# Optimization experiments

Hardware: AMD Instinct MI355X
Metric: run time of the kernel (lower is better)

## Reference

```python
import jax, jax.numpy as jnp
import numpy as np

WINDOW_SIZE = 11
SIGMA = 1.5
C3 = 1e-4
EPS = 1e-12


def _gaussian_window(channels):
    # 1D Gaussian, normalized, then outer product -> 2D separable window
    coords = jnp.arange(WINDOW_SIZE, dtype=jnp.float32) - WINDOW_SIZE // 2
    g = jnp.exp(-coords ** 2 / (2.0 * SIGMA ** 2))
    g = g / g.sum()
    w2 = g[:, None] * g[None, :]                      # [K, K]
    return jnp.broadcast_to(w2, (channels, 1, WINDOW_SIZE, WINDOW_SIZE))


def _dwconv(x, w, channels):
    # depthwise (groups=C) 2D conv with SAME-style symmetric zero padding
    pad = WINDOW_SIZE // 2
    return jax.lax.conv_general_dilated(
        x, w,
        window_strides=(1, 1),
        padding=[(pad, pad), (pad, pad)],
        dimension_numbers=('NCHW', 'OIHW', 'NCHW'),
        feature_group_count=channels,
    )


def reference(x, y):
    x = x.astype(jnp.float32)
    y = y.astype(jnp.float32)
    N, C = x.shape[0], x.shape[1]
    w = _gaussian_window(C)
    mu_x = _dwconv(x, w, C)
    mu_y = _dwconv(y, w, C)
    sigma_xy = _dwconv(x * y, w, C) - mu_x * mu_y
    sigma_x = jnp.clip(_dwconv(x * x, w, C) - mu_x * mu_x, EPS, None)
    sigma_y = jnp.clip(_dwconv(y * y, w, C) - mu_y * mu_y, EPS, None)
    structure = (sigma_xy + C3) / (jnp.sqrt(sigma_x) * jnp.sqrt(sigma_y) + C3)
    structure_mean = structure.reshape(N, C, -1).mean(axis=2)  # [N, C]
    loss = (1.0 - structure_mean).mean()
    return loss


def setup_inputs() -> dict:
    key = jax.random.key(0)
    kx, ky = jax.random.split(key)
    x = jax.random.uniform(kx, (8, 3, 512, 512), dtype=jnp.float32)
    y = jax.random.uniform(ky, (8, 3, 512, 512), dtype=jnp.float32)
    return {"x": x, "y": y}
```

## Files before the change

### kernel.cpp

```cpp
#include <hip/hip_runtime.h>

#define IMG 512
#define ROWS 8
#define NITER 18
#define NPLANES 24
#define TOTAL_PIX 6291456.0f
#define NBLOCKS (64 * 24)

__device__ __constant__ float GW[11] = {
    0.00102838f, 0.00759876f, 0.03600050f, 0.10935817f, 0.21300535f,
    0.26601172f, 0.21300535f, 0.10935817f, 0.03600050f, 0.00759876f,
    0.00102838f};

#define VSTRIDE 264
#define QSTRIDE 528
#define LDS_F2 2640

extern "C" __global__ __launch_bounds__(256, 4) void ssim_structure_kernel(
    const float* __restrict__ x, const float* __restrict__ y,
    float* __restrict__ partial) {
  const int tid = threadIdx.x;
  const int chunk = blockIdx.x;
  const int plane = blockIdx.y;
  const int r0 = chunk * ROWS;

  const size_t pbase = (size_t)plane * (IMG * IMG / 2);
  const float2* __restrict__ xp = (const float2*)x + pbase;
  const float2* __restrict__ yp = (const float2*)y + pbase;

  __shared__ float2 vbuf[LDS_F2];
  for (int j = tid; j < LDS_F2; j += 256) vbuf[j] = make_float2(0.f, 0.f);
  __syncthreads();

  float bx0[11], bx1[11], by0[11], by1[11];
  float acc = 0.0f;

  auto loadrow = [&](int i, float2& ox, float2& oy) {
    const int ir = r0 - 5 + i;
    if (i < NITER && ir >= 0 && ir < IMG) {
      const size_t off = (size_t)ir * (IMG / 2) + tid;
      ox = xp[off];
      oy = yp[off];
    } else {
      ox = make_float2(0.f, 0.f);
      oy = make_float2(0.f, 0.f);
    }
  };

#pragma unroll
  for (int i = 0; i < 10; ++i) {
    float2 vx, vy;
    loadrow(i, vx, vy);
    bx0[i] = vx.x;
    bx1[i] = vx.y;
    by0[i] = vy.x;
    by1[i] = vy.y;
  }
  float2 px, py;
  loadrow(10, px, py);

#pragma unroll
  for (int j = 0; j < ROWS; ++j) {
    const int slot = (10 + j) % 11;
    const int sel = j & 1;
    bx0[slot] = px.x;
    bx1[slot] = px.y;
    by0[slot] = py.x;
    by1[slot] = py.y;
    loadrow(11 + j, px, py);

    float Vx0 = 0.f, Vx1 = 0.f, Vy0 = 0.f, Vy1 = 0.f;
    float Vxx0 = 0.f, Vxx1 = 0.f, Vyy0 = 0.f, Vyy1 = 0.f;
    float Vxy0 = 0.f, Vxy1 = 0.f;
#pragma unroll
    for (int k = 0; k < 11; ++k) {
      const int s = (j + k) % 11;
      const float wgt = GW[k];
      const float wx0 = wgt * bx0[s], wx1 = wgt * bx1[s];
      const float wy0 = wgt * by0[s], wy1 = wgt * by1[s];
      Vx0 += wx0;
      Vx1 += wx1;
      Vy0 += wy0;
      Vy1 += wy1;
      Vxx0 = fmaf(wx0, bx0[s], Vxx0);
      Vxx1 = fmaf(wx1, bx1[s], Vxx1);
      Vxy0 = fmaf(wx0, by0[s], Vxy0);
      Vxy1 = fmaf(wx1, by1[s], Vxy1);
      Vyy0 = fmaf(wy0, by0[s], Vyy0);
      Vyy1 = fmaf(wy1, by1[s], Vyy1);
    }
    const int wbase = sel * VSTRIDE + 3 + tid;
    vbuf[0 * QSTRIDE + wbase] = make_float2(Vx0, Vx1);
    vbuf[1 * QSTRIDE + wbase] = make_float2(Vy0, Vy1);
    vbuf[2 * QSTRIDE + wbase] = make_float2(Vxx0, Vxx1);
    vbuf[3 * QSTRIDE + wbase] = make_float2(Vyy0, Vyy1);
    vbuf[4 * QSTRIDE + wbase] = make_float2(Vxy0, Vxy1);
    __syncthreads();

    float S0[5], S1[5];
#pragma unroll
    for (int q = 0; q < 5; ++q) {
      const float2* arr = vbuf + q * QSTRIDE + sel * VSTRIDE + tid;
      float a[14];
#pragma unroll
      for (int d = 0; d < 7; ++d) {
        const float2 v = arr[d];
        a[2 * d] = v.x;
        a[2 * d + 1] = v.y;
      }
      float s0 = 0.f, s1 = 0.f;
#pragma unroll
      for (int d = 0; d < 11; ++d) {
        s0 = fmaf(GW[d], a[d + 1], s0);
        s1 = fmaf(GW[d], a[d + 2], s1);
      }
      S0[q] = s0;
      S1[q] = s1;
    }
    {
      const float mx = S0[0], my = S0[1];
      const float sxy = fmaf(-mx, my, S0[4]);
      const float sxx = fmaxf(fmaf(-mx, mx, S0[2]), 1e-12f);
      const float syy = fmaxf(fmaf(-my, my, S0[3]), 1e-12f);
      const float den = __builtin_amdgcn_sqrtf(sxx * syy) + 1e-4f;
      acc += (sxy + 1e-4f) * __builtin_amdgcn_rcpf(den);
    }
    {
      const float mx = S1[0], my = S1[1];
      const float sxy = fmaf(-mx, my, S1[4]);
      const float sxx = fmaxf(fmaf(-mx, mx, S1[2]), 1e-12f);
      const float syy = fmaxf(fmaf(-my, my, S1[3]), 1e-12f);
      const float den = __builtin_amdgcn_sqrtf(sxx * syy) + 1e-4f;
      acc += (sxy + 1e-4f) * __builtin_amdgcn_rcpf(den);
    }
  }

#pragma unroll
  for (int off = 32; off > 0; off >>= 1) acc += __shfl_down(acc, off, 64);
  __shared__ float wsum[4];
  if ((tid & 63) == 0) wsum[tid >> 6] = acc;
  __syncthreads();
  if (tid == 0) {
    partial[blockIdx.y * 64 + blockIdx.x] = wsum[0] + wsum[1] + wsum[2] + wsum[3];
  }
}

extern "C" __global__ void ssim_finalize_kernel(const float* __restrict__ partial,
                                                float* __restrict__ out) {
  const int tid = threadIdx.x;
  float s = 0.f;
  for (int j = tid; j < NBLOCKS; j += 256) s += partial[j];
#pragma unroll
  for (int off = 32; off > 0; off >>= 1) s += __shfl_down(s, off, 64);
  __shared__ float wsum[4];
  if ((tid & 63) == 0) wsum[tid >> 6] = s;
  __syncthreads();
  if (tid == 0) {
    out[0] = 1.0f - (wsum[0] + wsum[1] + wsum[2] + wsum[3]) * (1.0f / TOTAL_PIX);
  }
}

extern "C" void kernel_launch(void* const* d_in, const int* in_sizes, int n_in,
                              void* d_out, int out_size, void* d_ws,
                              size_t ws_size, hipStream_t stream) {
  const float* x = (const float*)d_in[0];
  const float* y = (const float*)d_in[1];
  float* out = (float*)d_out;
  float* partial = (float*)d_ws;

  dim3 grid(IMG / ROWS, NPLANES, 1);
  ssim_structure_kernel<<<grid, 256, 0, stream>>>(x, y, partial);
  ssim_finalize_kernel<<<1, 256, 0, stream>>>(partial, out);
}
```

Before: 134.6 us.

## Double rows per block, pack LDS intermediates as float4, inline weights

Each block now processes 16 output rows instead of 8, which halves the number of blocks and lowers the fraction of redundant halo row loads. The vertical-pass results are packed into float4/float2 LDS arrays so the horizontal pass issues wider, fewer LDS reads. Gaussian weights become compile-time constants instead of constant-memory loads. The full manual unroll over 16 rows raises code size and register pressure, and halving the grid gives the GPU less parallelism to spread across its compute units.

```diff
diff --git a/kernel.cpp b/kernel.cpp
--- a/kernel.cpp
+++ b/kernel.cpp
@@ -1,20 +1,89 @@
 #include <hip/hip_runtime.h>
 
 #define IMG 512
-#define ROWS 8
-#define NITER 18
+#define ROWS 16
+#define NITER 26
 #define NPLANES 24
 #define TOTAL_PIX 6291456.0f
-#define NBLOCKS (64 * 24)
-
-__device__ __constant__ float GW[11] = {
+#define NBLOCKS (32 * 24)
+
+constexpr float GW[11] = {
     0.00102838f, 0.00759876f, 0.03600050f, 0.10935817f, 0.21300535f,
     0.26601172f, 0.21300535f, 0.10935817f, 0.03600050f, 0.00759876f,
     0.00102838f};
 
-#define VSTRIDE 264
-#define QSTRIDE 528
-#define LDS_F2 2640
+__device__ __forceinline__ void vcol(
+    float x0, float x1, float x2, float x3, float x4, float x5, float x6,
+    float x7, float x8, float x9, float x10,
+    float y0, float y1, float y2, float y3, float y4, float y5, float y6,
+    float y7, float y8, float y9, float y10,
+    float& Vx, float& Vy, float& Vxx, float& Vyy, float& Vxy) {
+  Vx = 0.f; Vy = 0.f; Vxx = 0.f; Vyy = 0.f; Vxy = 0.f;
+#define VK(K)                                            \
+  {                                                      \
+    const float wx = GW[K] * x##K, wy = GW[K] * y##K;    \
+    Vx += wx;                                            \
+    Vy += wy;                                            \
+    Vxx = fmaf(wx, x##K, Vxx);                           \
+    Vxy = fmaf(wx, y##K, Vxy);                           \
+    Vyy = fmaf(wy, y##K, Vyy);                           \
+  }
+  VK(0) VK(1) VK(2) VK(3) VK(4) VK(5) VK(6) VK(7) VK(8) VK(9) VK(10)
+#undef VK
+}
+
+__device__ __forceinline__ void hconv4(
+    const float4 p0, const float4 p1, const float4 p2, const float4 p3,
+    const float4 p4, const float4 p5, const float4 p6,
+    float& s0a, float& s1a, float& s0b, float& s1b) {
+  s0a = GW[0] * p0.y;
+  s0a = fmaf(GW[1], p1.x, s0a); s0a = fmaf(GW[2], p1.y, s0a);
+  s0a = fmaf(GW[3], p2.x, s0a); s0a = fmaf(GW[4], p2.y, s0a);
+  s0a = fmaf(GW[5], p3.x, s0a); s0a = fmaf(GW[6], p3.y, s0a);
+  s0a = fmaf(GW[7], p4.x, s0a); s0a = fmaf(GW[8], p4.y, s0a);
+  s0a = fmaf(GW[9], p5.x, s0a); s0a = fmaf(GW[10], p5.y, s0a);
+  s1a = GW[0] * p1.x;
+  s1a = fmaf(GW[1], p1.y, s1a); s1a = fmaf(GW[2], p2.x, s1a);
+  s1a = fmaf(GW[3], p2.y, s1a); s1a = fmaf(GW[4], p3.x, s1a);
+  s1a = fmaf(GW[5], p3.y, s1a); s1a = fmaf(GW[6], p4.x, s1a);
+  s1a = fmaf(GW[7], p4.y, s1a); s1a = fmaf(GW[8], p5.x, s1a);
+  s1a = fmaf(GW[9], p5.y, s1a); s1a = fmaf(GW[10], p6.x, s1a);
+  s0b = GW[0] * p0.w;
+  s0b = fmaf(GW[1], p1.z, s0b); s0b = fmaf(GW[2], p1.w, s0b);
+  s0b = fmaf(GW[3], p2.z, s0b); s0b = fmaf(GW[4], p2.w, s0b);
+  s0b = fmaf(GW[5], p3.z, s0b); s0b = fmaf(GW[6], p3.w, s0b);
+  s0b = fmaf(GW[7], p4.z, s0b); s0b = fmaf(GW[8], p4.w, s0b);
+  s0b = fmaf(GW[9], p5.z, s0b); s0b = fmaf(GW[10], p5.w, s0b);
+  s1b = GW[0] * p1.z;
+  s1b = fmaf(GW[1], p1.w, s1b); s1b = fmaf(GW[2], p2.z, s1b);
+  s1b = fmaf(GW[3], p2.w, s1b); s1b = fmaf(GW[4], p3.z, s1b);
+  s1b = fmaf(GW[5], p3.w, s1b); s1b = fmaf(GW[6], p4.z, s1b);
+  s1b = fmaf(GW[7], p4.w, s1b); s1b = fmaf(GW[8], p5.z, s1b);
+  s1b = fmaf(GW[9], p5.w, s1b); s1b = fmaf(GW[10], p6.z, s1b);
+}
+
+__device__ __forceinline__ void hconv2(
+    const float2 q0, const float2 q1, const float2 q2, const float2 q3,
+    const float2 q4, const float2 q5, const float2 q6, float& s0, float& s1) {
+  s0 = GW[0] * q0.y;
+  s0 = fmaf(GW[1], q1.x, s0); s0 = fmaf(GW[2], q1.y, s0);
+  s0 = fmaf(GW[3], q2.x, s0); s0 = fmaf(GW[4], q2.y, s0);
+  s0 = fmaf(GW[5], q3.x, s0); s0 = fmaf(GW[6], q3.y, s0);
+  s0 = fmaf(GW[7], q4.x, s0); s0 = fmaf(GW[8], q4.y, s0);
+  s0 = fmaf(GW[9], q5.x, s0); s0 = fmaf(GW[10], q5.y, s0);
+  s1 = GW[0] * q1.x;
+  s1 = fmaf(GW[1], q1.y, s1); s1 = fmaf(GW[2], q2.x, s1);
+  s1 = fmaf(GW[3], q2.y, s1); s1 = fmaf(GW[4], q3.x, s1);
+  s1 = fmaf(GW[5], q3.y, s1); s1 = fmaf(GW[6], q4.x, s1);
+  s1 = fmaf(GW[7], q4.y, s1); s1 = fmaf(GW[8], q5.x, s1);
+  s1 = fmaf(GW[9], q5.y, s1); s1 = fmaf(GW[10], q6.x, s1);
+}
+
+#define ROTA(A, J)                                                          \
+  A[((J) + 0) % 11], A[((J) + 1) % 11], A[((J) + 2) % 11],                  \
+  A[((J) + 3) % 11], A[((J) + 4) % 11], A[((J) + 5) % 11],                  \
+  A[((J) + 6) % 11], A[((J) + 7) % 11], A[((J) + 8) % 11],                  \
+  A[((J) + 9) % 11], A[((J) + 10) % 11]
 
 extern "C" __global__ __launch_bounds__(256, 4) void ssim_structure_kernel(
     const float* __restrict__ x, const float* __restrict__ y,
@@ -28,8 +97,14 @@
   const float2* __restrict__ xp = (const float2*)x + pbase;
   const float2* __restrict__ yp = (const float2*)y + pbase;
 
-  __shared__ float2 vbuf[LDS_F2];
-  for (int j = tid; j < LDS_F2; j += 256) vbuf[j] = make_float2(0.f, 0.f);
+  __shared__ float4 b01[2][264];
+  __shared__ float4 b23[2][264];
+  __shared__ float2 b4[2][264];
+  for (int j = tid; j < 528; j += 256) {
+    ((float4*)b01)[j] = make_float4(0.f, 0.f, 0.f, 0.f);
+    ((float4*)b23)[j] = make_float4(0.f, 0.f, 0.f, 0.f);
+    ((float2*)b4)[j] = make_float2(0.f, 0.f);
+  }
   __syncthreads();
 
   float bx0[11], bx1[11], by0[11], by1[11];
@@ -47,93 +122,60 @@
     }
   };
 
-#pragma unroll
-  for (int i = 0; i < 10; ++i) {
-    float2 vx, vy;
-    loadrow(i, vx, vy);
-    bx0[i] = vx.x;
-    bx1[i] = vx.y;
-    by0[i] = vy.x;
-    by1[i] = vy.y;
-  }
+#define LOADP(I)                                             \
+  {                                                          \
+    float2 vx, vy;                                           \
+    loadrow(I, vx, vy);                                      \
+    bx0[I] = vx.x; bx1[I] = vx.y;                            \
+    by0[I] = vy.x; by1[I] = vy.y;                            \
+  }
+  LOADP(0) LOADP(1) LOADP(2) LOADP(3) LOADP(4)
+  LOADP(5) LOADP(6) LOADP(7) LOADP(8) LOADP(9)
+#undef LOADP
   float2 px, py;
   loadrow(10, px, py);
 
-#pragma unroll
-  for (int j = 0; j < ROWS; ++j) {
-    const int slot = (10 + j) % 11;
-    const int sel = j & 1;
-    bx0[slot] = px.x;
-    bx1[slot] = px.y;
-    by0[slot] = py.x;
-    by1[slot] = py.y;
-    loadrow(11 + j, px, py);
-
-    float Vx0 = 0.f, Vx1 = 0.f, Vy0 = 0.f, Vy1 = 0.f;
-    float Vxx0 = 0.f, Vxx1 = 0.f, Vyy0 = 0.f, Vyy1 = 0.f;
-    float Vxy0 = 0.f, Vxy1 = 0.f;
-#pragma unroll
-    for (int k = 0; k < 11; ++k) {
-      const int s = (j + k) % 11;
-      const float wgt = GW[k];
-      const float wx0 = wgt * bx0[s], wx1 = wgt * bx1[s];
-      const float wy0 = wgt * by0[s], wy1 = wgt * by1[s];
-      Vx0 += wx0;
-      Vx1 += wx1;
-      Vy0 += wy0;
-      Vy1 += wy1;
-      Vxx0 = fmaf(wx0, bx0[s], Vxx0);
-      Vxx1 = fmaf(wx1, bx1[s], Vxx1);
-      Vxy0 = fmaf(wx0, by0[s], Vxy0);
-      Vxy1 = fmaf(wx1, by1[s], Vxy1);
-      Vyy0 = fmaf(wy0, by0[s], Vyy0);
-      Vyy1 = fmaf(wy1, by1[s], Vyy1);
-    }
-    const int wbase = sel * VSTRIDE + 3 + tid;
-    vbuf[0 * QSTRIDE + wbase] = make_float2(Vx0, Vx1);
-    vbuf[1 * QSTRIDE + wbase] = make_float2(Vy0, Vy1);
-    vbuf[2 * QSTRIDE + wbase] = make_float2(Vxx0, Vxx1);
-    vbuf[3 * QSTRIDE + wbase] = make_float2(Vyy0, Vyy1);
-    vbuf[4 * QSTRIDE + wbase] = make_float2(Vxy0, Vxy1);
-    __syncthreads();
-
-    float S0[5], S1[5];
-#pragma unroll
-    for (int q = 0; q < 5; ++q) {
-      const float2* arr = vbuf + q * QSTRIDE + sel * VSTRIDE + tid;
-      float a[14];
-#pragma unroll
-      for (int d = 0; d < 7; ++d) {
-        const float2 v = arr[d];
-        a[2 * d] = v.x;
-        a[2 * d + 1] = v.y;
-      }
-      float s0 = 0.f, s1 = 0.f;
-#pragma unroll
-      for (int d = 0; d < 11; ++d) {
-        s0 = fmaf(GW[d], a[d + 1], s0);
-        s1 = fmaf(GW[d], a[d + 2], s1);
-      }
-      S0[q] = s0;
-      S1[q] = s1;
-    }
-    {
-      const float mx = S0[0], my = S0[1];
-      const float sxy = fmaf(-mx, my, S0[4]);
-      const float sxx = fmaxf(fmaf(-mx, mx, S0[2]), 1e-12f);
-      const float syy = fmaxf(fmaf(-my, my, S0[3]), 1e-12f);
-      const float den = __builtin_amdgcn_sqrtf(sxx * syy) + 1e-4f;
-      acc += (sxy + 1e-4f) * __builtin_amdgcn_rcpf(den);
-    }
-    {
-      const float mx = S1[0], my = S1[1];
-      const float sxy = fmaf(-mx, my, S1[4]);
-      const float sxx = fmaxf(fmaf(-mx, mx, S1[2]), 1e-12f);
-      const float syy = fmaxf(fmaf(-my, my, S1[3]), 1e-12f);
-      const float den = __builtin_amdgcn_sqrtf(sxx * syy) + 1e-4f;
-      acc += (sxy + 1e-4f) * __builtin_amdgcn_rcpf(den);
-    }
-  }
+#define STEP(J)                                                               \
+  {                                                                           \
+    bx0[(10 + (J)) % 11] = px.x; bx1[(10 + (J)) % 11] = px.y;                 \
+    by0[(10 + (J)) % 11] = py.x; by1[(10 + (J)) % 11] = py.y;                 \
+    loadrow(11 + (J), px, py);                                                \
+    float Vx0, Vy0, Vxx0, Vyy0, Vxy0, Vx1, Vy1, Vxx1, Vyy1, Vxy1;            \
+    vcol(ROTA(bx0, J), ROTA(by0, J), Vx0, Vy0, Vxx0, Vyy0, Vxy0);             \
+    vcol(ROTA(bx1, J), ROTA(by1, J), Vx1, Vy1, Vxx1, Vyy1, Vxy1);             \
+    const int sel = (J) & 1;                                                  \
+    b01[sel][3 + tid] = make_float4(Vx0, Vx1, Vy0, Vy1);                      \
+    b23[sel][3 + tid] = make_float4(Vxx0, Vxx1, Vyy0, Vyy1);                  \
+    b4[sel][3 + tid] = make_float2(Vxy0, Vxy1);                               \
+    __syncthreads();                                                          \
+    float Sx0, Sx1, Sy0, Sy1, Sxx0, Sxx1, Syy0, Syy1, Sxy0, Sxy1;            \
+    hconv4(b01[sel][tid], b01[sel][tid + 1], b01[sel][tid + 2],               \
+           b01[sel][tid + 3], b01[sel][tid + 4], b01[sel][tid + 5],           \
+           b01[sel][tid + 6], Sx0, Sx1, Sy0, Sy1);                            \
+    hconv4(b23[sel][tid], b23[sel][tid + 1], b23[sel][tid + 2],               \
+           b23[sel][tid + 3], b23[sel][tid + 4], b23[sel][tid + 5],           \
+           b23[sel][tid + 6], Sxx0, Sxx1, Syy0, Syy1);                        \
+    hconv2(b4[sel][tid], b4[sel][tid + 1], b4[sel][tid + 2],                  \
+           b4[sel][tid + 3], b4[sel][tid + 4], b4[sel][tid + 5],              \
+           b4[sel][tid + 6], Sxy0, Sxy1);                                     \
+    {                                                                         \
+      const float sxy = fmaf(-Sx0, Sy0, Sxy0);                                \
+      const float sxx = fmaxf(fmaf(-Sx0, Sx0, Sxx0), 1e-12f);                 \
+      const float syy = fmaxf(fmaf(-Sy0, Sy0, Syy0), 1e-12f);                 \
+      const float den = __builtin_amdgcn_sqrtf(sxx * syy) + 1e-4f;            \
+      acc += (sxy + 1e-4f) * __builtin_amdgcn_rcpf(den);                      \
+    }                                                                         \
+    {                                                                         \
+      const float sxy = fmaf(-Sx1, Sy1, Sxy1);                                \
+      const float sxx = fmaxf(fmaf(-Sx1, Sx1, Sxx1), 1e-12f);                 \
+      const float syy = fmaxf(fmaf(-Sy1, Sy1, Syy1), 1e-12f);                 \
+      const float den = __builtin_amdgcn_sqrtf(sxx * syy) + 1e-4f;            \
+      acc += (sxy + 1e-4f) * __builtin_amdgcn_rcpf(den);                      \
+    }                                                                         \
+  }
+  STEP(0) STEP(1) STEP(2) STEP(3) STEP(4) STEP(5) STEP(6) STEP(7)
+  STEP(8) STEP(9) STEP(10) STEP(11) STEP(12) STEP(13) STEP(14) STEP(15)
+#undef STEP
 
 #pragma unroll
   for (int off = 32; off > 0; off >>= 1) acc += __shfl_down(acc, off, 64);
@@ -141,7 +183,8 @@
   if ((tid & 63) == 0) wsum[tid >> 6] = acc;
   __syncthreads();
   if (tid == 0) {
-    partial[blockIdx.y * 64 + blockIdx.x] = wsum[0] + wsum[1] + wsum[2] + wsum[3];
+    partial[blockIdx.y * 32 + blockIdx.x] =
+        wsum[0] + wsum[1] + wsum[2] + wsum[3];
   }
 }
 
```

Measured after the change: 407.6 us. +202.8%, slower.
